# Kernel optimization log

Hardware: AMD Instinct MI355X
Metric: run time of the kernel (lower is better)

The kernel has to match this reference:

```python
import jax, jax.numpy as jnp
import numpy as np

B, T, H = 2048, 512, 64  # batch, seq_len, hidden_size


def setup_inputs() -> dict:
    key = jax.random.key(0)
    ks = jax.random.split(key, 12)
    s = 1.0 / np.sqrt(H)  # PyTorch default uniform init bound
    u = lambda k, shape: jax.random.uniform(k, shape, jnp.float32, -s, s)
    return {
        "x": jax.random.normal(ks[0], (B, T), dtype=jnp.float32),
        # layer 0: input_size=1
        "w_ih0": u(ks[1], (4 * H, 1)),
        "w_hh0": u(ks[2], (4 * H, H)),
        "b_ih0": u(ks[3], (4 * H,)),
        "b_hh0": u(ks[4], (4 * H,)),
        # layer 1: input_size=H
        "w_ih1": u(ks[5], (4 * H, H)),
        "w_hh1": u(ks[6], (4 * H, H)),
        "b_ih1": u(ks[7], (4 * H,)),
        "b_hh1": u(ks[8], (4 * H,)),
        # final projection 64 -> 1
        "fc_w": u(ks[9], (1, H)),
        "fc_b": u(ks[10], (1,)),
    }


def _lstm_layer(x, w_ih, w_hh, b_ih, b_hh):
    """x: [B, T, D] -> hidden states [B, T, H]. PyTorch gate order i,f,g,o."""
    bsz = x.shape[0]
    # input contribution for all timesteps at once: [B, T, 4H]
    gx = jnp.einsum('btd,gd->btg', x, w_ih) + b_ih + b_hh
    gx = jnp.swapaxes(gx, 0, 1)  # time-major [T, B, 4H]

    def step(carry, g_t):
        h, c = carry
        g = g_t + h @ w_hh.T  # [B, 4H]
        i, f, gg, o = jnp.split(g, 4, axis=-1)
        i = jax.nn.sigmoid(i)
        f = jax.nn.sigmoid(f)
        gg = jnp.tanh(gg)
        o = jax.nn.sigmoid(o)
        c = f * c + i * gg
        h = o * jnp.tanh(c)
        return (h, c), h

    h0 = jnp.zeros((bsz, H), dtype=x.dtype)
    _, hs = jax.lax.scan(step, (h0, h0), gx)
    return jnp.swapaxes(hs, 0, 1)  # [B, T, H]


def reference(x, w_ih0, w_hh0, b_ih0, b_hh0, w_ih1, w_hh1, b_ih1, b_hh1, fc_w, fc_b):
    x3 = x[..., None]  # unsqueeze(2): [B, T, 1]
    h1 = _lstm_layer(x3, w_ih0, w_hh0, b_ih0, b_hh0)
    h2 = _lstm_layer(h1, w_ih1, w_hh1, b_ih1, b_hh1)
    # fc applied to last timestep of layer-2 output
    return h2[:, -1, :] @ fc_w.T + fc_b  # [B, 1]
```

## Files before the change

kernel.cpp:

```cpp
#include <hip/hip_runtime.h>

#define TLEN 512
#define HDIM 64
#define NB   8
#define NTH  512
#define GRID 256
#define XPAD 740

typedef __attribute__((ext_vector_type(8))) short bf16x8;
typedef __attribute__((ext_vector_type(4))) short short4v;
typedef __attribute__((ext_vector_type(4))) float f32x4;

__device__ __forceinline__ float sigm(float x){ return __fdividef(1.f, 1.f+__expf(-x)); }
__device__ __forceinline__ float tanh_(float x){ return 1.f - __fdividef(2.f, __expf(2.f*x)+1.f); }

__device__ __forceinline__ short bf16rn(float f){
    unsigned u = __float_as_uint(f);
    u = (u + 0x7FFFu + ((u >> 16) & 1u)) >> 16;
    return (short)u;
}
__device__ __forceinline__ float bf2f(short s){
    return __uint_as_float(((unsigned)(unsigned short)s) << 16);
}

__device__ __forceinline__ void loadA(const float* __restrict__ W, int rowbase, int lane,
                                      bf16x8& hi0, bf16x8& lo0, bf16x8& hi1, bf16x8& lo1)
{
    const int row = rowbase + (lane & 15);
    const int q   = lane >> 4;
    const float* p = W + row * HDIM + q * 8;
    #pragma unroll
    for (int e = 0; e < 8; ++e) {
        const float f0 = p[e];
        const float f1 = p[32 + e];
        const short a0 = bf16rn(f0); hi0[e] = a0; lo0[e] = bf16rn(f0 - bf2f(a0));
        const short a1 = bf16rn(f1); hi1[e] = a1; lo1[e] = bf16rn(f1 - bf2f(a1));
    }
}

#define MFMA __builtin_amdgcn_mfma_f32_16x16x32_bf16

__global__ __launch_bounds__(NTH, 1)
void lstm2_ws(const float* __restrict__ x,
              const float* __restrict__ w_ih0,
              const float* __restrict__ w_hh0,
              const float* __restrict__ b_ih0,
              const float* __restrict__ b_hh0,
              const float* __restrict__ w_ih1,
              const float* __restrict__ w_hh1,
              const float* __restrict__ b_ih1,
              const float* __restrict__ b_hh1,
              const float* __restrict__ fc_w,
              const float* __restrict__ fc_b,
              float* __restrict__ out)
{
    __shared__ float xs[16 * XPAD];
    __shared__ short h1f[2][2][2][4][16][8];
    __shared__ short h2f[2][2][2][4][16][8];
    __shared__ float h2last[16][HDIM];

    const int tid  = threadIdx.x;
    const int wid  = tid >> 6;
    const int lane = tid & 63;
    const int q    = lane >> 4;
    const int r15  = lane & 15;
    const int b0   = blockIdx.x * NB;
    const bool isL0 = (wid < 4);

    {
        const float4* xg = (const float4*)(x + (size_t)b0 * TLEN);
        for (int idx = tid; idx < 16 * TLEN / 4; idx += NTH) {
            const int row = idx >> 7;
            const int col = idx & 127;
            *(float4*)&xs[row * XPAD + col * 4] = xg[(row & 7) * 128 + col];
        }
    }
    for (int idx = tid; idx < 8192; idx += NTH) {
        ((short*)h1f)[idx] = 0;
        ((short*)h2f)[idx] = 0;
    }

    const int w4 = isL0 ? wid : (wid - 4);
    const int U0 = w4 * 16;
    bf16x8 M0h0[4], M0l0[4], M0h1[4], M0l1[4];
    bf16x8 M1h0[4], M1l0[4], M1h1[4], M1l1[4];
    f32x4 biasv[4], wih[4];
    if (isL0) {
        #pragma unroll
        for (int g = 0; g < 4; ++g)
            loadA(w_hh0, g * 64 + U0, lane, M0h0[g], M0l0[g], M0h1[g], M0l1[g]);
        #pragma unroll
        for (int g = 0; g < 4; ++g) {
            #pragma unroll
            for (int r = 0; r < 4; ++r) {
                const int row = g * 64 + U0 + q * 4 + r;
                biasv[g][r] = b_ih0[row] + b_hh0[row];
                wih[g][r]   = w_ih0[row];
            }
        }
    } else {
        #pragma unroll
        for (int g = 0; g < 4; ++g) {
            loadA(w_ih1, g * 64 + U0, lane, M0h0[g], M0l0[g], M0h1[g], M0l1[g]);
            loadA(w_hh1, g * 64 + U0, lane, M1h0[g], M1l0[g], M1h1[g], M1l1[g]);
        }
        #pragma unroll
        for (int g = 0; g < 4; ++g) {
            #pragma unroll
            for (int r = 0; r < 4; ++r) {
                const int row = g * 64 + U0 + q * 4 + r;
                biasv[g][r] = b_ih1[row] + b_hh1[row];
                wih[g][r]   = 0.f;
            }
        }
    }
    const int kh = w4 >> 1;
    const int qp = (2 * w4 + (q >> 1)) & 3;
    const int eo = (q & 1) * 4;
    f32x4 cc = {0.f, 0.f, 0.f, 0.f};
    int p = 0;

    __syncthreads();

    for (int i = 0; i <= TLEN; ++i) {
        const bool active = isL0 ? (i < TLEN) : (i >= 1);
        if (active) {
            f32x4 acc[4];
            if (isL0) {
                const bf16x8 Bh0 = *(const bf16x8*)&h1f[p][0][0][q][r15][0];
                const bf16x8 Bh1 = *(const bf16x8*)&h1f[p][0][1][q][r15][0];
                const bf16x8 Bl0 = *(const bf16x8*)&h1f[p][1][0][q][r15][0];
                const bf16x8 Bl1 = *(const bf16x8*)&h1f[p][1][1][q][r15][0];
                const float xv = xs[r15 * XPAD + i];
                #pragma unroll
                for (int g = 0; g < 4; ++g) {
                    f32x4 a = biasv[g];
                    #pragma unroll
                    for (int r = 0; r < 4; ++r) a[r] = fmaf(wih[g][r], xv, a[r]);
                    a = MFMA(M0h0[g], Bh0, a, 0, 0, 0);
                    a = MFMA(M0h1[g], Bh1, a, 0, 0, 0);
                    a = MFMA(M0l0[g], Bh0, a, 0, 0, 0);
                    a = MFMA(M0l1[g], Bh1, a, 0, 0, 0);
                    a = MFMA(M0h0[g], Bl0, a, 0, 0, 0);
                    a = MFMA(M0h1[g], Bl1, a, 0, 0, 0);
                    acc[g] = a;
                }
            } else {
                const bf16x8 B1h0 = *(const bf16x8*)&h1f[p][0][0][q][r15][0];
                const bf16x8 B1h1 = *(const bf16x8*)&h1f[p][0][1][q][r15][0];
                const bf16x8 B1l0 = *(const bf16x8*)&h1f[p][1][0][q][r15][0];
                const bf16x8 B1l1 = *(const bf16x8*)&h1f[p][1][1][q][r15][0];
                const bf16x8 B2h0 = *(const bf16x8*)&h2f[p][0][0][q][r15][0];
                const bf16x8 B2h1 = *(const bf16x8*)&h2f[p][0][1][q][r15][0];
                const bf16x8 B2l0 = *(const bf16x8*)&h2f[p][1][0][q][r15][0];
                const bf16x8 B2l1 = *(const bf16x8*)&h2f[p][1][1][q][r15][0];
                #pragma unroll
                for (int g = 0; g < 4; ++g) {
                    f32x4 a = biasv[g];
                    a = MFMA(M0h0[g], B1h0, a, 0, 0, 0);
                    a = MFMA(M0h1[g], B1h1, a, 0, 0, 0);
                    a = MFMA(M0l0[g], B1h0, a, 0, 0, 0);
                    a = MFMA(M0l1[g], B1h1, a, 0, 0, 0);
                    a = MFMA(M0h0[g], B1l0, a, 0, 0, 0);
                    a = MFMA(M0h1[g], B1l1, a, 0, 0, 0);
                    f32x4 h = {0.f, 0.f, 0.f, 0.f};
                    h = MFMA(M1h0[g], B2h0, h, 0, 0, 0);
                    h = MFMA(M1h1[g], B2h1, h, 0, 0, 0);
                    h = MFMA(M1l0[g], B2h0, h, 0, 0, 0);
                    h = MFMA(M1l1[g], B2h1, h, 0, 0, 0);
                    h = MFMA(M1h0[g], B2l0, h, 0, 0, 0);
                    h = MFMA(M1h1[g], B2l1, h, 0, 0, 0);
                    #pragma unroll
                    for (int r = 0; r < 4; ++r) acc[g][r] = a[r] + h[r];
                }
            }
            float hv[4];
            #pragma unroll
            for (int r = 0; r < 4; ++r) {
                const float gi = sigm (acc[0][r]);
                const float gf = sigm (acc[1][r]);
                const float gg = tanh_(acc[2][r]);
                const float go = sigm (acc[3][r]);
                cc[r] = fmaf(gf, cc[r], gi * gg);
                hv[r] = go * tanh_(cc[r]);
            }
            const short hh0 = bf16rn(hv[0]), hl0 = bf16rn(hv[0] - bf2f(hh0));
            const short hh1 = bf16rn(hv[1]), hl1 = bf16rn(hv[1] - bf2f(hh1));
            const short hh2 = bf16rn(hv[2]), hl2 = bf16rn(hv[2] - bf2f(hh2));
            const short hh3 = bf16rn(hv[3]), hl3 = bf16rn(hv[3] - bf2f(hh3));
            if (isL0) {
                *(short4v*)&h1f[p ^ 1][0][kh][qp][r15][eo] = (short4v){hh0, hh1, hh2, hh3};
                *(short4v*)&h1f[p ^ 1][1][kh][qp][r15][eo] = (short4v){hl0, hl1, hl2, hl3};
            } else {
                *(short4v*)&h2f[p ^ 1][0][kh][qp][r15][eo] = (short4v){hh0, hh1, hh2, hh3};
                *(short4v*)&h2f[p ^ 1][1][kh][qp][r15][eo] = (short4v){hl0, hl1, hl2, hl3};
                if (i == TLEN)
                    *(f32x4*)&h2last[r15][U0 + q * 4] = (f32x4){hv[0], hv[1], hv[2], hv[3]};
            }
        }
        __syncthreads();
        p ^= 1;
    }

    {
        const int fb = tid >> 5, fs = tid & 31;
        float psum = fc_w[fs] * h2last[fb][fs] + fc_w[fs + 32] * h2last[fb][fs + 32];
        psum += __shfl_xor(psum, 16);
        psum += __shfl_xor(psum, 8);
        psum += __shfl_xor(psum, 4);
        psum += __shfl_xor(psum, 2);
        psum += __shfl_xor(psum, 1);
        if (fs == 0 && fb < NB) out[b0 + fb] = psum + fc_b[0];
    }
}

extern "C" void kernel_launch(void* const* d_in, const int* in_sizes, int n_in,
                              void* d_out, int out_size, void* d_ws, size_t ws_size,
                              hipStream_t stream) {
    const float* xp     = (const float*)d_in[0];
    const float* w_ih0  = (const float*)d_in[1];
    const float* w_hh0  = (const float*)d_in[2];
    const float* b_ih0  = (const float*)d_in[3];
    const float* b_hh0  = (const float*)d_in[4];
    const float* w_ih1  = (const float*)d_in[5];
    const float* w_hh1  = (const float*)d_in[6];
    const float* b_ih1  = (const float*)d_in[7];
    const float* b_hh1  = (const float*)d_in[8];
    const float* fc_w   = (const float*)d_in[9];
    const float* fc_b   = (const float*)d_in[10];
    float* outp = (float*)d_out;

    lstm2_ws<<<dim3(GRID), dim3(NTH), 0, stream>>>(
        xp, w_ih0, w_hh0, b_ih0, b_hh0,
        w_ih1, w_hh1, b_ih1, b_hh1, fc_w, fc_b, outp);
}
```

Measured before the change: 1.061 ms.

## Split gate nonlinearities across lane halves, shuffle results, allow two waves per EU

Rows of the batch tile 8-15 are padding, so each lane now evaluates the LSTM cell for only two of its four accumulator rows, picking the two relevant rows by lane half. The packed bf16 hi/lo results are exchanged with a lane-xor-8 shuffle to rebuild the full store. The 6-MFMA dependency chain in layer 0 is split into two independent 3-MFMA chains, the x smem padding is reduced, and the launch attribute allows two waves per EU. This halves the transcendental work per step and shortens MFMA latency chains, at the cost of extra shuffles and possible register pressure from the occupancy hint.

```diff
diff --git a/kernel.cpp b/kernel.cpp
--- a/kernel.cpp
+++ b/kernel.cpp
@@ -5,10 +5,9 @@
 #define NB   8
 #define NTH  512
 #define GRID 256
-#define XPAD 740
+#define XPAD 516
 
 typedef __attribute__((ext_vector_type(8))) short bf16x8;
-typedef __attribute__((ext_vector_type(4))) short short4v;
 typedef __attribute__((ext_vector_type(4))) float f32x4;
 
 __device__ __forceinline__ float sigm(float x){ return __fdividef(1.f, 1.f+__expf(-x)); }
@@ -21,6 +20,9 @@
 }
 __device__ __forceinline__ float bf2f(short s){
     return __uint_as_float(((unsigned)(unsigned short)s) << 16);
+}
+__device__ __forceinline__ float bf2f_u(unsigned lo16){
+    return __uint_as_float(lo16 << 16);
 }
 
 __device__ __forceinline__ void loadA(const float* __restrict__ W, int rowbase, int lane,
@@ -40,7 +42,8 @@
 
 #define MFMA __builtin_amdgcn_mfma_f32_16x16x32_bf16
 
-__global__ __launch_bounds__(NTH, 1)
+__global__ __launch_bounds__(NTH)
+__attribute__((amdgpu_waves_per_eu(2, 2)))
 void lstm2_ws(const float* __restrict__ x,
               const float* __restrict__ w_ih0,
               const float* __restrict__ w_hh0,
@@ -65,7 +68,8 @@
     const int q    = lane >> 4;
     const int r15  = lane & 15;
     const int b0   = blockIdx.x * NB;
-    const bool isL0 = (wid < 4);
+    const bool isL0   = (wid < 4);
+    const bool lohalf = (r15 < 8);
 
     {
         const float4* xg = (const float4*)(x + (size_t)b0 * TLEN);
@@ -117,7 +121,7 @@
     const int kh = w4 >> 1;
     const int qp = (2 * w4 + (q >> 1)) & 3;
     const int eo = (q & 1) * 4;
-    f32x4 cc = {0.f, 0.f, 0.f, 0.f};
+    float ccA = 0.f, ccB = 0.f;
     int p = 0;
 
     __syncthreads();
@@ -138,12 +142,14 @@
                     #pragma unroll
                     for (int r = 0; r < 4; ++r) a[r] = fmaf(wih[g][r], xv, a[r]);
                     a = MFMA(M0h0[g], Bh0, a, 0, 0, 0);
-                    a = MFMA(M0h1[g], Bh1, a, 0, 0, 0);
                     a = MFMA(M0l0[g], Bh0, a, 0, 0, 0);
-                    a = MFMA(M0l1[g], Bh1, a, 0, 0, 0);
                     a = MFMA(M0h0[g], Bl0, a, 0, 0, 0);
-                    a = MFMA(M0h1[g], Bl1, a, 0, 0, 0);
-                    acc[g] = a;
+                    f32x4 b2 = {0.f, 0.f, 0.f, 0.f};
+                    b2 = MFMA(M0h1[g], Bh1, b2, 0, 0, 0);
+                    b2 = MFMA(M0l1[g], Bh1, b2, 0, 0, 0);
+                    b2 = MFMA(M0h1[g], Bl1, b2, 0, 0, 0);
+                    #pragma unroll
+                    for (int r = 0; r < 4; ++r) acc[g][r] = a[r] + b2[r];
                 }
             } else {
                 const bf16x8 B1h0 = *(const bf16x8*)&h1f[p][0][0][q][r15][0];
@@ -174,28 +180,49 @@
                     for (int r = 0; r < 4; ++r) acc[g][r] = a[r] + h[r];
                 }
             }
-            float hv[4];
+            float a0g[4], a1g[4];
             #pragma unroll
-            for (int r = 0; r < 4; ++r) {
-                const float gi = sigm (acc[0][r]);
-                const float gf = sigm (acc[1][r]);
-                const float gg = tanh_(acc[2][r]);
-                const float go = sigm (acc[3][r]);
-                cc[r] = fmaf(gf, cc[r], gi * gg);
-                hv[r] = go * tanh_(cc[r]);
-            }
-            const short hh0 = bf16rn(hv[0]), hl0 = bf16rn(hv[0] - bf2f(hh0));
-            const short hh1 = bf16rn(hv[1]), hl1 = bf16rn(hv[1] - bf2f(hh1));
-            const short hh2 = bf16rn(hv[2]), hl2 = bf16rn(hv[2] - bf2f(hh2));
-            const short hh3 = bf16rn(hv[3]), hl3 = bf16rn(hv[3] - bf2f(hh3));
+            for (int g = 0; g < 4; ++g) {
+                a0g[g] = lohalf ? acc[g][0] : acc[g][2];
+                a1g[g] = lohalf ? acc[g][1] : acc[g][3];
+            }
+            float hvA, hvB;
+            {
+                const float gi = sigm(a0g[0]), gf = sigm(a0g[1]);
+                const float gg = tanh_(a0g[2]), go = sigm(a0g[3]);
+                ccA = fmaf(gf, ccA, gi * gg);
+                hvA = go * tanh_(ccA);
+            }
+            {
+                const float gi = sigm(a1g[0]), gf = sigm(a1g[1]);
+                const float gg = tanh_(a1g[2]), go = sigm(a1g[3]);
+                ccB = fmaf(gf, ccB, gi * gg);
+                hvB = go * tanh_(ccB);
+            }
+            const short sA = bf16rn(hvA), lA = bf16rn(hvA - bf2f(sA));
+            const short sB = bf16rn(hvB), lB = bf16rn(hvB - bf2f(sB));
+            const unsigned ownH = (unsigned)(unsigned short)sA | ((unsigned)(unsigned short)sB << 16);
+            const unsigned ownL = (unsigned)(unsigned short)lA | ((unsigned)(unsigned short)lB << 16);
+            const unsigned othH = (unsigned)__shfl_xor((int)ownH, 8, 64);
+            const unsigned othL = (unsigned)__shfl_xor((int)ownL, 8, 64);
+            const unsigned h01 = lohalf ? ownH : othH;
+            const unsigned h23 = lohalf ? othH : ownH;
+            const unsigned l01 = lohalf ? ownL : othL;
+            const unsigned l23 = lohalf ? othL : ownL;
             if (isL0) {
-                *(short4v*)&h1f[p ^ 1][0][kh][qp][r15][eo] = (short4v){hh0, hh1, hh2, hh3};
-                *(short4v*)&h1f[p ^ 1][1][kh][qp][r15][eo] = (short4v){hl0, hl1, hl2, hl3};
+                *(uint2*)&h1f[p ^ 1][0][kh][qp][r15][eo] = (uint2){h01, h23};
+                *(uint2*)&h1f[p ^ 1][1][kh][qp][r15][eo] = (uint2){l01, l23};
             } else {
-                *(short4v*)&h2f[p ^ 1][0][kh][qp][r15][eo] = (short4v){hh0, hh1, hh2, hh3};
-                *(short4v*)&h2f[p ^ 1][1][kh][qp][r15][eo] = (short4v){hl0, hl1, hl2, hl3};
-                if (i == TLEN)
-                    *(f32x4*)&h2last[r15][U0 + q * 4] = (f32x4){hv[0], hv[1], hv[2], hv[3]};
+                *(uint2*)&h2f[p ^ 1][0][kh][qp][r15][eo] = (uint2){h01, h23};
+                *(uint2*)&h2f[p ^ 1][1][kh][qp][r15][eo] = (uint2){l01, l23};
+                if (i == TLEN) {
+                    f32x4 hv;
+                    hv[0] = bf2f_u(h01 & 0xFFFFu) + bf2f_u(l01 & 0xFFFFu);
+                    hv[1] = bf2f_u(h01 >> 16)     + bf2f_u(l01 >> 16);
+                    hv[2] = bf2f_u(h23 & 0xFFFFu) + bf2f_u(l23 & 0xFFFFu);
+                    hv[3] = bf2f_u(h23 >> 16)     + bf2f_u(l23 >> 16);
+                    *(f32x4*)&h2last[r15][U0 + q * 4] = hv;
+                }
             }
         }
         __syncthreads();
```

New measurement: 872.8 us. -17.7%, faster.
